# Kernel tuning notes

Measured on AMD Instinct MI355X. Metric: run time of the kernel, lower is better.

The kernel has to match this reference:

```python
import jax, jax.numpy as jnp
import numpy as np

D = 768      # model dim
E = 8        # n_experts
S = 2        # slots_per_expert
B, N = 8, 4096


def setup_inputs() -> dict:
    key = jax.random.key(0)
    ks = jax.random.split(key, 6)
    x   = jax.random.normal(ks[0], (B, N, D), dtype=jnp.float32)
    phi = jax.random.normal(ks[1], (D, E * S), dtype=jnp.float32)
    # per-expert FFN params, stacked over experts (fan-in scaled init)
    w1 = jax.random.normal(ks[2], (E, D, 4 * D), dtype=jnp.float32) * (1.0 / np.sqrt(D))
    b1 = jnp.zeros((E, 4 * D), dtype=jnp.float32)
    w2 = jax.random.normal(ks[3], (E, 4 * D, D), dtype=jnp.float32) * (1.0 / np.sqrt(4 * D))
    b2 = jnp.zeros((E, D), dtype=jnp.float32)
    return {"x": x, "phi": phi, "w1": w1, "b1": b1, "w2": w2, "b2": b2}


def reference(x, phi, w1, b1, w2, b2):
    # logits: [B, N, E*S]
    logits = jnp.einsum('bnd,de->bne', x, phi)
    dispatch = jax.nn.softmax(logits, axis=-1)   # over slots
    combine  = jax.nn.softmax(logits, axis=1)    # over tokens
    # dispatch: weighted average of tokens per slot -> [B, E*S, D]
    xs = jnp.einsum('bne,bnd->bed', dispatch, x)
    xs = xs.reshape(B, E, S, D)
    # grouped per-expert FFN (exact/erf GELU, matching torch nn.GELU default)
    h  = jax.nn.gelu(jnp.einsum('besd,edf->besf', xs, w1) + b1[:, None, :], approximate=False)
    ys = jnp.einsum('besf,efd->besd', h, w2) + b2[:, None, :]
    ys = ys.reshape(B, E * S, D)
    # combine: [B, N, E*S] @ [B, E*S, D] -> [B, N, D]
    y = jnp.einsum('bne,bed->bnd', combine, ys)
    return y
```

## Files before the change

kernel.cpp:

```cpp
#include <hip/hip_runtime.h>
#include <math.h>

#define BB 8
#define NN 4096
#define DD 768
#define EE 8
#define SS 2
#define ES 16
#define FF 3072


__global__ __launch_bounds__(256) void k_logits(const float* __restrict__ x,
                                                const float* __restrict__ phi,
                                                float* __restrict__ logits,
                                                float* __restrict__ disp) {
  __shared__ float part[4][64][20];
  const int tid = threadIdx.x;
  const int b   = blockIdx.x >> 6;
  const int n0  = (blockIdx.x & 63) * 64;
  const int w   = __builtin_amdgcn_readfirstlane(tid >> 6);
  const int l   = tid & 63;

  const float* xr  = x + (size_t)(b * NN + n0 + l) * DD + 192 * w;
  const float* pr0 = phi + 192 * w * ES;

  float acc[16];
  #pragma unroll
  for (int j = 0; j < 16; ++j) acc[j] = 0.f;

  #pragma unroll 2
  for (int k = 0; k < 48; ++k) {
    const float4 xv = *(const float4*)(xr + 4 * k);
    const float* pr = pr0 + 4 * k * ES;
    #pragma unroll
    for (int j = 0; j < 16; ++j) {
      acc[j] += xv.x * pr[j] + xv.y * pr[ES + j] + xv.z * pr[2 * ES + j] +
                xv.w * pr[3 * ES + j];
    }
  }
  #pragma unroll
  for (int q = 0; q < 4; ++q)
    ((float4*)part[w][l])[q] =
        make_float4(acc[4 * q], acc[4 * q + 1], acc[4 * q + 2], acc[4 * q + 3]);
  __syncthreads();

  const int t  = tid >> 2;
  const int jq = tid & 3;
  float4 s = ((const float4*)part[0][t])[jq];
  #pragma unroll
  for (int ww = 1; ww < 4; ++ww) {
    const float4 p = ((const float4*)part[ww][t])[jq];
    s.x += p.x; s.y += p.y; s.z += p.z; s.w += p.w;
  }
  float m = fmaxf(fmaxf(s.x, s.y), fmaxf(s.z, s.w));
  m = fmaxf(m, __shfl_xor(m, 1));
  m = fmaxf(m, __shfl_xor(m, 2));
  float4 ev = make_float4(__expf(s.x - m), __expf(s.y - m), __expf(s.z - m),
                          __expf(s.w - m));
  float sum = ev.x + ev.y + ev.z + ev.w;
  sum += __shfl_xor(sum, 1);
  sum += __shfl_xor(sum, 2);
  const float inv = 1.f / sum;
  const size_t base = (size_t)(b * NN + n0 + t) * ES + jq * 4;
  *(float4*)(logits + base) = s;
  *(float4*)(disp + base) =
      make_float4(ev.x * inv, ev.y * inv, ev.z * inv, ev.w * inv);
}

__global__ __launch_bounds__(128) void k_cpart(const float* __restrict__ logits,
                                               float* __restrict__ mpart,
                                               float* __restrict__ spart) {
  __shared__ float4 red[128][4];
  const int b   = blockIdx.x >> 5;
  const int ch  = blockIdx.x & 31;
  const int tid = threadIdx.x;
  const size_t base = (size_t)(b * NN + ch * 128 + tid) * ES;

  float4 v[4];
  #pragma unroll
  for (int q = 0; q < 4; ++q) v[q] = *(const float4*)(logits + base + 4 * q);
  #pragma unroll
  for (int q = 0; q < 4; ++q) red[tid][q] = v[q];
  __syncthreads();
  for (int s = 64; s > 0; s >>= 1) {
    if (tid < s) {
      #pragma unroll
      for (int q = 0; q < 4; ++q) {
        float4 a = red[tid][q], o = red[tid + s][q];
        a.x = fmaxf(a.x, o.x); a.y = fmaxf(a.y, o.y);
        a.z = fmaxf(a.z, o.z); a.w = fmaxf(a.w, o.w);
        red[tid][q] = a;
      }
    }
    __syncthreads();
  }
  float4 mx[4];
  #pragma unroll
  for (int q = 0; q < 4; ++q) mx[q] = red[0][q];
  __syncthreads();

  #pragma unroll
  for (int q = 0; q < 4; ++q)
    red[tid][q] = make_float4(__expf(v[q].x - mx[q].x), __expf(v[q].y - mx[q].y),
                              __expf(v[q].z - mx[q].z), __expf(v[q].w - mx[q].w));
  __syncthreads();
  for (int s = 64; s > 0; s >>= 1) {
    if (tid < s) {
      #pragma unroll
      for (int q = 0; q < 4; ++q) {
        float4 a = red[tid][q], o = red[tid + s][q];
        a.x += o.x; a.y += o.y; a.z += o.z; a.w += o.w;
        red[tid][q] = a;
      }
    }
    __syncthreads();
  }
  if (tid == 0) {
    const int ob = (b * 32 + ch) * ES;
    #pragma unroll
    for (int q = 0; q < 4; ++q) {
      *(float4*)(mpart + ob + 4 * q) = mx[q];
      *(float4*)(spart + ob + 4 * q) = red[0][q];
    }
  }
}

__global__ __launch_bounds__(64) void k_cfin(const float* __restrict__ mpart,
                                             const float* __restrict__ spart,
                                             float* __restrict__ cmax,
                                             float* __restrict__ cinv) {
  const int b = blockIdx.x;
  const int j = threadIdx.x;
  if (j < 16) {
    float m = -1e30f;
    #pragma unroll 4
    for (int c = 0; c < 32; ++c)
      m = fmaxf(m, mpart[(b * 32 + c) * ES + j]);
    float S = 0.f;
    #pragma unroll 4
    for (int c = 0; c < 32; ++c)
      S += spart[(b * 32 + c) * ES + j] * __expf(mpart[(b * 32 + c) * ES + j] - m);
    cmax[b * ES + j] = m;
    cinv[b * ES + j] = 1.f / S;
  }
}

__global__ __launch_bounds__(192) void k_xsA(const float* __restrict__ x,
                                             const float* __restrict__ disp,
                                             float* __restrict__ xspart) {
  const int b   = blockIdx.x >> 6;
  const int n0  = (blockIdx.x & 63) * 64;
  const int tid = threadIdx.x;

  float4 acc[16];
  #pragma unroll
  for (int e = 0; e < 16; ++e) acc[e] = make_float4(0.f, 0.f, 0.f, 0.f);

  #pragma unroll 4
  for (int t = 0; t < 64; ++t) {
    const size_t tb = (size_t)(b * NN + n0 + t);
    const float4 xv = *(const float4*)(x + tb * DD + 4 * tid);
    const float* dp = disp + tb * ES;
    #pragma unroll
    for (int e = 0; e < 16; ++e) {
      const float wgt = dp[e];
      acc[e].x += wgt * xv.x; acc[e].y += wgt * xv.y;
      acc[e].z += wgt * xv.z; acc[e].w += wgt * xv.w;
    }
  }
  #pragma unroll
  for (int e = 0; e < 16; ++e)
    *(float4*)(xspart + ((size_t)blockIdx.x * 16 + e) * DD + 4 * tid) = acc[e];
}

__global__ __launch_bounds__(256) void k_xsB(const float* __restrict__ xspart,
                                             float* __restrict__ xs) {
  const int q4  = blockIdx.x * 256 + threadIdx.x;
  const int row = q4 / 192;
  const int c4  = q4 % 192;
  const int b   = row >> 4;
  const int e   = row & 15;
  float4 s = make_float4(0.f, 0.f, 0.f, 0.f);
  #pragma unroll 8
  for (int p = 0; p < 64; ++p) {
    const float4 v =
        *(const float4*)(xspart + (((size_t)(b * 64 + p)) * 16 + e) * DD + 4 * c4);
    s.x += v.x; s.y += v.y; s.z += v.z; s.w += v.w;
  }
  *(float4*)(xs + (size_t)row * DD + 4 * c4) = s;
}

__global__ __launch_bounds__(256) void k_ffn1(const float* __restrict__ xs,
                                              const float* __restrict__ w1,
                                              float* __restrict__ hpart) {
  const int bid  = blockIdx.x;
  const int e    = bid / 96;
  const int fblk = (bid / 8) % 12;
  const int dp   = bid % 8;
  const int tid  = threadIdx.x;
  const int f    = fblk * 256 + 4 * (tid & 63);
  const int sg   = __builtin_amdgcn_readfirstlane(tid >> 6);

  const float* xr[4];
  #pragma unroll
  for (int i = 0; i < 4; ++i) {
    const int r = 4 * sg + i;
    xr[i] = xs + (size_t)((r >> 1) * ES + e * SS + (r & 1)) * DD + dp * 96;
  }
  const float* wp = w1 + (size_t)e * DD * FF + (size_t)(dp * 96) * FF + f;

  float4 acc[4];
  #pragma unroll
  for (int i = 0; i < 4; ++i) acc[i] = make_float4(0.f, 0.f, 0.f, 0.f);

  #pragma unroll 4
  for (int dd = 0; dd < 96; ++dd) {
    const float4 wv = *(const float4*)(wp + (size_t)dd * FF);
    #pragma unroll
    for (int i = 0; i < 4; ++i) {
      const float xv = xr[i][dd];
      acc[i].x += xv * wv.x; acc[i].y += xv * wv.y;
      acc[i].z += xv * wv.z; acc[i].w += xv * wv.w;
    }
  }
  #pragma unroll
  for (int i = 0; i < 4; ++i)
    *(float4*)(hpart + ((size_t)dp * 128 + e * 16 + 4 * sg + i) * FF + f) = acc[i];
}

__global__ __launch_bounds__(256) void k_gelu(const float* __restrict__ hpart,
                                              const float* __restrict__ b1,
                                              float* __restrict__ h) {
  const int q4  = blockIdx.x * 256 + threadIdx.x;
  const int row = q4 / 768;
  const int c4  = q4 % 768;
  const int e   = row >> 4;
  float4 s = make_float4(0.f, 0.f, 0.f, 0.f);
  #pragma unroll
  for (int dp = 0; dp < 8; ++dp) {
    const float4 v = *(const float4*)(hpart + ((size_t)dp * 128 + row) * FF + 4 * c4);
    s.x += v.x; s.y += v.y; s.z += v.z; s.w += v.w;
  }
  const float4 bb = *(const float4*)(b1 + e * FF + 4 * c4);
  const float ks = 0.70710678118654752f;
  float a;
  float4 o;
  a = s.x + bb.x; o.x = 0.5f * a * (1.f + erff(a * ks));
  a = s.y + bb.y; o.y = 0.5f * a * (1.f + erff(a * ks));
  a = s.z + bb.z; o.z = 0.5f * a * (1.f + erff(a * ks));
  a = s.w + bb.w; o.w = 0.5f * a * (1.f + erff(a * ks));
  *(float4*)(h + (size_t)row * FF + 4 * c4) = o;
}

__global__ __launch_bounds__(256) void k_ffn2(const float* __restrict__ h,
                                              const float* __restrict__ w2,
                                              float* __restrict__ yspart) {
  const int bid  = blockIdx.x;
  const int e    = bid / 96;
  const int dblk = (bid / 32) % 3;
  const int fp   = bid % 32;
  const int tid  = threadIdx.x;
  const int dcol = dblk * 256 + 4 * (tid & 63);
  const int sg   = __builtin_amdgcn_readfirstlane(tid >> 6);
  const int f0   = fp * 96;

  const float* hr[4];
  #pragma unroll
  for (int i = 0; i < 4; ++i)
    hr[i] = h + (size_t)(e * 16 + 4 * sg + i) * FF + f0;
  const float* wp = w2 + (size_t)e * FF * DD + (size_t)f0 * DD + dcol;

  float4 acc[4];
  #pragma unroll
  for (int i = 0; i < 4; ++i) acc[i] = make_float4(0.f, 0.f, 0.f, 0.f);

  #pragma unroll 4
  for (int ff = 0; ff < 96; ++ff) {
    const float4 wv = *(const float4*)(wp + (size_t)ff * DD);
    #pragma unroll
    for (int i = 0; i < 4; ++i) {
      const float hv = hr[i][ff];
      acc[i].x += hv * wv.x; acc[i].y += hv * wv.y;
      acc[i].z += hv * wv.z; acc[i].w += hv * wv.w;
    }
  }
  #pragma unroll
  for (int i = 0; i < 4; ++i)
    *(float4*)(yspart + ((size_t)fp * 128 + e * 16 + 4 * sg + i) * DD + dcol) = acc[i];
}

__global__ __launch_bounds__(256) void k_ysred(const float* __restrict__ yspart,
                                               const float* __restrict__ b2,
                                               float* __restrict__ ys) {
  const int q4  = blockIdx.x * 256 + threadIdx.x;
  const int q   = q4 / 192;
  const int c4  = q4 % 192;
  const int b   = q >> 4;
  const int es  = q & 15;
  const int e   = es >> 1;
  const int s   = es & 1;
  const int prow = e * 16 + b * 2 + s;
  float4 acc = *(const float4*)(b2 + e * DD + 4 * c4);
  #pragma unroll 8
  for (int fp = 0; fp < 32; ++fp) {
    const float4 v = *(const float4*)(yspart + ((size_t)fp * 128 + prow) * DD + 4 * c4);
    acc.x += v.x; acc.y += v.y; acc.z += v.z; acc.w += v.w;
  }
  *(float4*)(ys + (size_t)q * DD + 4 * c4) = acc;
}

__global__ __launch_bounds__(192) void k_combine(const float* __restrict__ logits,
                                                 const float* __restrict__ ys,
                                                 const float* __restrict__ cmax,
                                                 const float* __restrict__ cinv,
                                                 float* __restrict__ y) {
  const int b   = blockIdx.x >> 6;
  const int n0  = (blockIdx.x & 63) * 64;
  const int tid = threadIdx.x;

  float4 ysr[16];
  float cm[16], ci[16];
  #pragma unroll
  for (int es = 0; es < 16; ++es) {
    cm[es] = cmax[b * ES + es];
    ci[es] = cinv[b * ES + es];
    ysr[es] = *(const float4*)(ys + (size_t)(b * ES + es) * DD + 4 * tid);
  }
  #pragma unroll 2
  for (int t = 0; t < 64; ++t) {
    const size_t tb = (size_t)(b * NN + n0 + t);
    const float* lp = logits + tb * ES;
    float4 a = make_float4(0.f, 0.f, 0.f, 0.f);
    #pragma unroll
    for (int es = 0; es < 16; ++es) {
      const float c = __expf(lp[es] - cm[es]) * ci[es];
      a.x += c * ysr[es].x; a.y += c * ysr[es].y;
      a.z += c * ysr[es].z; a.w += c * ysr[es].w;
    }
    *(float4*)(y + tb * DD + 4 * tid) = a;
  }
}

extern "C" void kernel_launch(void* const* d_in, const int* in_sizes, int n_in,
                              void* d_out, int out_size, void* d_ws, size_t ws_size,
                              hipStream_t stream) {
  const float* x   = (const float*)d_in[0];
  const float* phi = (const float*)d_in[1];
  const float* w1  = (const float*)d_in[2];
  const float* b1  = (const float*)d_in[3];
  const float* w2  = (const float*)d_in[4];
  const float* b2  = (const float*)d_in[5];
  float* y  = (float*)d_out;
  float* ws = (float*)d_ws;

  float* A      = ws;
  float* logits = ws + 6291456;
  float* disp   = ws + 6815744;
  float* xs     = ws + 7340032;
  float* h      = ws + 7438336;
  float* ys     = ws + 7831552;
  float* mpart  = ws + 7929856;
  float* spart  = ws + 7933952;
  float* cmax   = ws + 7938048;
  float* cinv   = ws + 7938176;

  hipLaunchKernelGGL(k_logits,  dim3(512), dim3(256), 0, stream, x, phi, logits, disp);
  hipLaunchKernelGGL(k_cpart,   dim3(256), dim3(128), 0, stream, logits, mpart, spart);
  hipLaunchKernelGGL(k_cfin,    dim3(8),   dim3(64),  0, stream, mpart, spart, cmax, cinv);
  hipLaunchKernelGGL(k_xsA,     dim3(512), dim3(192), 0, stream, x, disp, A);
  hipLaunchKernelGGL(k_xsB,     dim3(96),  dim3(256), 0, stream, A, xs);
  hipLaunchKernelGGL(k_ffn1,    dim3(768), dim3(256), 0, stream, xs, w1, A);
  hipLaunchKernelGGL(k_gelu,    dim3(384), dim3(256), 0, stream, A, b1, h);
  hipLaunchKernelGGL(k_ffn2,    dim3(768), dim3(256), 0, stream, h, w2, A);
  hipLaunchKernelGGL(k_ysred,   dim3(96),  dim3(256), 0, stream, A, b2, ys);
  hipLaunchKernelGGL(k_combine, dim3(512), dim3(192), 0, stream, logits, ys, cmax, cinv, y);
}
```

Before: 383.0 us.

## Fuse logits/dispatch softmax with slot aggregation, staging x tiles in LDS

```diff
diff --git a/kernel.cpp b/kernel.cpp
--- a/kernel.cpp
+++ b/kernel.cpp
@@ -10,61 +10,103 @@
 #define FF 3072
 
 
-__global__ __launch_bounds__(256) void k_logits(const float* __restrict__ x,
-                                                const float* __restrict__ phi,
-                                                float* __restrict__ logits,
-                                                float* __restrict__ disp) {
-  __shared__ float part[4][64][20];
-  const int tid = threadIdx.x;
-  const int b   = blockIdx.x >> 6;
-  const int n0  = (blockIdx.x & 63) * 64;
-  const int w   = __builtin_amdgcn_readfirstlane(tid >> 6);
-  const int l   = tid & 63;
-
-  const float* xr  = x + (size_t)(b * NN + n0 + l) * DD + 192 * w;
-  const float* pr0 = phi + 192 * w * ES;
-
-  float acc[16];
-  #pragma unroll
-  for (int j = 0; j < 16; ++j) acc[j] = 0.f;
-
-  #pragma unroll 2
-  for (int k = 0; k < 48; ++k) {
-    const float4 xv = *(const float4*)(xr + 4 * k);
-    const float* pr = pr0 + 4 * k * ES;
-    #pragma unroll
-    for (int j = 0; j < 16; ++j) {
-      acc[j] += xv.x * pr[j] + xv.y * pr[ES + j] + xv.z * pr[2 * ES + j] +
-                xv.w * pr[3 * ES + j];
-    }
-  }
-  #pragma unroll
-  for (int q = 0; q < 4; ++q)
-    ((float4*)part[w][l])[q] =
-        make_float4(acc[4 * q], acc[4 * q + 1], acc[4 * q + 2], acc[4 * q + 3]);
-  __syncthreads();
-
-  const int t  = tid >> 2;
-  const int jq = tid & 3;
-  float4 s = ((const float4*)part[0][t])[jq];
-  #pragma unroll
-  for (int ww = 1; ww < 4; ++ww) {
-    const float4 p = ((const float4*)part[ww][t])[jq];
-    s.x += p.x; s.y += p.y; s.z += p.z; s.w += p.w;
-  }
-  float m = fmaxf(fmaxf(s.x, s.y), fmaxf(s.z, s.w));
-  m = fmaxf(m, __shfl_xor(m, 1));
-  m = fmaxf(m, __shfl_xor(m, 2));
-  float4 ev = make_float4(__expf(s.x - m), __expf(s.y - m), __expf(s.z - m),
-                          __expf(s.w - m));
-  float sum = ev.x + ev.y + ev.z + ev.w;
-  sum += __shfl_xor(sum, 1);
-  sum += __shfl_xor(sum, 2);
-  const float inv = 1.f / sum;
-  const size_t base = (size_t)(b * NN + n0 + t) * ES + jq * 4;
-  *(float4*)(logits + base) = s;
-  *(float4*)(disp + base) =
-      make_float4(ev.x * inv, ev.y * inv, ev.z * inv, ev.w * inv);
+__global__ __launch_bounds__(512) void k_fused(const float* __restrict__ x,
+                                               const float* __restrict__ phi,
+                                               float* __restrict__ logits,
+                                               float* __restrict__ xspart) {
+  __shared__ float xt[32 * 768];
+  __shared__ float part[8][32][16];
+  __shared__ float dsp[32][16];
+
+  const int tid  = threadIdx.x;
+  const int b    = blockIdx.x >> 6;
+  const int grp  = blockIdx.x & 63;
+  const int n0   = grp * 64;
+  const int w    = tid >> 6;
+  const int lane = tid & 63;
+  const int j    = lane & 15;
+  const int uu   = lane >> 4;
+  const int d0   = 96 * w + 24 * uu;
+  const int g    = w >> 2;
+  const int wsub = w & 3;
+  const bool xact = (wsub < 3);
+  const int d4   = wsub * 64 + lane;
+
+  float preg[24];
+  #pragma unroll
+  for (int k = 0; k < 24; ++k) preg[k] = phi[(d0 + k) * ES + j];
+
+  float4 acc[8];
+  #pragma unroll
+  for (int i = 0; i < 8; ++i) acc[i] = make_float4(0.f, 0.f, 0.f, 0.f);
+
+  for (int tile = 0; tile < 2; ++tile) {
+    const int nt = n0 + tile * 32;
+
+    #pragma unroll
+    for (int i = 0; i < 12; ++i) {
+      const int f4 = tid + i * 512;
+      const int r  = f4 / 192, c = f4 % 192;
+      *(float4*)(xt + r * 768 + 4 * c) =
+          *(const float4*)(x + ((size_t)(b * NN + nt + r)) * DD + 4 * c);
+    }
+    __syncthreads();
+
+    for (int t = 0; t < 32; ++t) {
+      float p = 0.f;
+      #pragma unroll
+      for (int i4 = 0; i4 < 6; ++i4) {
+        const float4 xv = *(const float4*)(xt + t * 768 + d0 + 4 * i4);
+        p += xv.x * preg[4 * i4] + xv.y * preg[4 * i4 + 1] +
+             xv.z * preg[4 * i4 + 2] + xv.w * preg[4 * i4 + 3];
+      }
+      p += __shfl_xor(p, 16);
+      p += __shfl_xor(p, 32);
+      if (uu == 0) part[w][t][j] = p;
+    }
+    __syncthreads();
+
+    {
+      const int t = tid >> 4, jj = tid & 15;
+      float s = 0.f;
+      #pragma unroll
+      for (int ww = 0; ww < 8; ++ww) s += part[ww][t][jj];
+      float m = s;
+      m = fmaxf(m, __shfl_xor(m, 1));
+      m = fmaxf(m, __shfl_xor(m, 2));
+      m = fmaxf(m, __shfl_xor(m, 4));
+      m = fmaxf(m, __shfl_xor(m, 8));
+      const float ev = __expf(s - m);
+      float sum = ev;
+      sum += __shfl_xor(sum, 1);
+      sum += __shfl_xor(sum, 2);
+      sum += __shfl_xor(sum, 4);
+      sum += __shfl_xor(sum, 8);
+      logits[((size_t)(b * NN + nt + t)) * ES + jj] = s;
+      dsp[t][jj] = ev * (1.f / sum);
+    }
+    __syncthreads();
+
+    if (xact) {
+      for (int t = 0; t < 32; ++t) {
+        const float4 xv = *(const float4*)(xt + t * 768 + 4 * d4);
+        #pragma unroll
+        for (int i = 0; i < 8; ++i) {
+          const float dw = dsp[t][8 * g + i];
+          acc[i].x += dw * xv.x; acc[i].y += dw * xv.y;
+          acc[i].z += dw * xv.z; acc[i].w += dw * xv.w;
+        }
+      }
+    }
+    __syncthreads();
+  }
+
+  if (xact) {
+    #pragma unroll
+    for (int i = 0; i < 8; ++i)
+      *(float4*)(xspart + (((size_t)(b * 64 + grp)) * 16 + 8 * g + i) * DD +
+                 4 * d4) = acc[i];
+  }
 }
 
 __global__ __launch_bounds__(128) void k_cpart(const float* __restrict__ logits,
@@ -145,34 +187,6 @@
   }
 }
 
-__global__ __launch_bounds__(192) void k_xsA(const float* __restrict__ x,
-                                             const float* __restrict__ disp,
-                                             float* __restrict__ xspart) {
-  const int b   = blockIdx.x >> 6;
-  const int n0  = (blockIdx.x & 63) * 64;
-  const int tid = threadIdx.x;
-
-  float4 acc[16];
-  #pragma unroll
-  for (int e = 0; e < 16; ++e) acc[e] = make_float4(0.f, 0.f, 0.f, 0.f);
-
-  #pragma unroll 4
-  for (int t = 0; t < 64; ++t) {
-    const size_t tb = (size_t)(b * NN + n0 + t);
-    const float4 xv = *(const float4*)(x + tb * DD + 4 * tid);
-    const float* dp = disp + tb * ES;
-    #pragma unroll
-    for (int e = 0; e < 16; ++e) {
-      const float wgt = dp[e];
-      acc[e].x += wgt * xv.x; acc[e].y += wgt * xv.y;
-      acc[e].z += wgt * xv.z; acc[e].w += wgt * xv.w;
-    }
-  }
-  #pragma unroll
-  for (int e = 0; e < 16; ++e)
-    *(float4*)(xspart + ((size_t)blockIdx.x * 16 + e) * DD + 4 * tid) = acc[e];
-}
-
 __global__ __launch_bounds__(256) void k_xsB(const float* __restrict__ xspart,
                                              float* __restrict__ xs) {
   const int q4  = blockIdx.x * 256 + threadIdx.x;
@@ -355,19 +369,17 @@
 
   float* A      = ws;
   float* logits = ws + 6291456;
-  float* disp   = ws + 6815744;
-  float* xs     = ws + 7340032;
-  float* h      = ws + 7438336;
-  float* ys     = ws + 7831552;
-  float* mpart  = ws + 7929856;
-  float* spart  = ws + 7933952;
-  float* cmax   = ws + 7938048;
-  float* cinv   = ws + 7938176;
-
-  hipLaunchKernelGGL(k_logits,  dim3(512), dim3(256), 0, stream, x, phi, logits, disp);
+  float* xs     = ws + 6815744;
+  float* h      = ws + 6914048;
+  float* ys     = ws + 7307264;
+  float* mpart  = ws + 7405568;
+  float* spart  = ws + 7409664;
+  float* cmax   = ws + 7413760;
+  float* cinv   = ws + 7413888;
+
+  hipLaunchKernelGGL(k_fused,   dim3(512), dim3(512), 0, stream, x, phi, logits, A);
   hipLaunchKernelGGL(k_cpart,   dim3(256), dim3(128), 0, stream, logits, mpart, spart);
   hipLaunchKernelGGL(k_cfin,    dim3(8),   dim3(64),  0, stream, mpart, spart, cmax, cinv);
-  hipLaunchKernelGGL(k_xsA,     dim3(512), dim3(192), 0, stream, x, disp, A);
   hipLaunchKernelGGL(k_xsB,     dim3(96),  dim3(256), 0, stream, A, xs);
   hipLaunchKernelGGL(k_ffn1,    dim3(768), dim3(256), 0, stream, xs, w1, A);
   hipLaunchKernelGGL(k_gelu,    dim3(384), dim3(256), 0, stream, A, b1, h);
```

After: 386.9 us. No clear change (+1.0%).
